# Kernel tuning notes

Hardware: AMD Instinct MI355X
Metric: run time of the kernel (lower is better)

Reference implementation:

```python
import jax, jax.numpy as jnp
import numpy as np

# 3D multi-scale deformable attention (MSDeformAttn, n_heads=8 / 3D variant)
LEVEL_SHAPES = [(32, 32, 32), (16, 16, 16), (8, 8, 8), (4, 4, 4)]  # (H, W, D) per level
D_MODEL, N_HEADS, N_LEVELS, N_POINTS = 256, 8, 4, 4
C_HEAD = D_MODEL // N_HEADS  # 32
N_BATCH, LEN_Q = 1, 37440
LEN_IN = sum(h * w * d for h, w, d in LEVEL_SHAPES)  # 37440


def setup_inputs() -> dict:
    key = jax.random.key(0)
    ks = jax.random.split(key, 10)
    s = 0.02  # param init scale
    return {
        "query": jax.random.normal(ks[0], (N_BATCH, LEN_Q, D_MODEL), jnp.float32),
        "reference_points": jax.random.uniform(ks[1], (N_BATCH, LEN_Q, N_LEVELS, 3), jnp.float32),
        "input_flatten": jax.random.normal(ks[2], (N_BATCH, LEN_IN, D_MODEL), jnp.float32),
        "input_spatial_shapes": jnp.array(LEVEL_SHAPES, dtype=jnp.int32),
        "input_level_start_index": jnp.array(
            np.cumsum([0] + [h * w * d for h, w, d in LEVEL_SHAPES])[:-1], dtype=jnp.int32),
        "W_value": s * jax.random.normal(ks[3], (D_MODEL, D_MODEL), jnp.float32),
        "b_value": jnp.zeros((D_MODEL,), jnp.float32),
        "W_off": s * jax.random.normal(ks[4], (D_MODEL, N_HEADS * N_LEVELS * N_POINTS * 3), jnp.float32),
        "b_off": s * jax.random.normal(ks[5], (N_HEADS * N_LEVELS * N_POINTS * 3,), jnp.float32),
        "W_attn": s * jax.random.normal(ks[6], (D_MODEL, N_HEADS * N_LEVELS * N_POINTS), jnp.float32),
        "b_attn": jnp.zeros((N_HEADS * N_LEVELS * N_POINTS,), jnp.float32),
        "W_out": s * jax.random.normal(ks[7], (D_MODEL, D_MODEL), jnp.float32),
        "b_out": jnp.zeros((D_MODEL,), jnp.float32),
    }


def trilinear_sample(vol, gx, gy, gz):
    """torch F.grid_sample 3D, mode=bilinear, padding=zeros, align_corners=False.
    vol: (B, C, Dz, Dy, Dx); gx indexes Dx, gy indexes Dy, gz indexes Dz, each (B, Q) in [-1,1].
    Returns (B, C, Q)."""
    B, C, Dz, Dy, Dx = vol.shape
    ix = ((gx + 1.0) * Dx - 1.0) * 0.5
    iy = ((gy + 1.0) * Dy - 1.0) * 0.5
    iz = ((gz + 1.0) * Dz - 1.0) * 0.5
    x0f, y0f, z0f = jnp.floor(ix), jnp.floor(iy), jnp.floor(iz)
    fx, fy, fz = ix - x0f, iy - y0f, iz - z0f
    x0, y0, z0 = x0f.astype(jnp.int32), y0f.astype(jnp.int32), z0f.astype(jnp.int32)
    vol_f = vol.reshape(B, C, Dz * Dy * Dx)
    out = jnp.zeros((B, C, gx.shape[1]), vol.dtype)
    for dz in (0, 1):
        for dy in (0, 1):
            for dx in (0, 1):
                xc, yc, zc = x0 + dx, y0 + dy, z0 + dz
                w = ((fx if dx else 1.0 - fx) * (fy if dy else 1.0 - fy) * (fz if dz else 1.0 - fz))
                valid = ((xc >= 0) & (xc < Dx) & (yc >= 0) & (yc < Dy) & (zc >= 0) & (zc < Dz))
                idx = (jnp.clip(zc, 0, Dz - 1) * Dy + jnp.clip(yc, 0, Dy - 1)) * Dx + jnp.clip(xc, 0, Dx - 1)
                v = jnp.take_along_axis(vol_f, idx[:, None, :], axis=2)  # (B, C, Q)
                out = out + (w * valid.astype(w.dtype))[:, None, :] * v
    return out


def reference(query, reference_points, input_flatten, input_spatial_shapes,
              input_level_start_index, W_value, b_value, W_off, b_off,
              W_attn, b_attn, W_out, b_out):
    N, Lq, _ = query.shape
    Lin = input_flatten.shape[1]
    value = (input_flatten @ W_value + b_value).reshape(N, Lin, N_HEADS, C_HEAD)
    off = (query @ W_off + b_off).reshape(N, Lq, N_HEADS, N_LEVELS, N_POINTS, 3)
    attn = jax.nn.softmax((query @ W_attn + b_attn).reshape(N, Lq, N_HEADS, N_LEVELS * N_POINTS), axis=-1)
    # offset_normalizer = [W, H, D] per level (as in the torch code)
    norm = jnp.stack([input_spatial_shapes[:, 1], input_spatial_shapes[:, 0],
                      input_spatial_shapes[:, 2]], -1).astype(query.dtype)
    loc = reference_points[:, :, None, :, None, :] + off / norm[None, None, None, :, None, :]
    grids = 2.0 * loc - 1.0  # (N, Lq, M, L, P, 3)
    starts = np.cumsum([0] + [h * w * d for h, w, d in LEVEL_SHAPES])
    sampled = []
    for l, (H, W, D) in enumerate(LEVEL_SHAPES):
        vl = value[:, starts[l]:starts[l + 1]]  # (N, H*W*D, M, C)
        vol = (vl.reshape(N, H, W, D, N_HEADS, C_HEAD)
                 .transpose(0, 4, 5, 1, 2, 3)
                 .reshape(N * N_HEADS, C_HEAD, H, W, D))
        g = grids[:, :, :, l].transpose(0, 2, 1, 3, 4).reshape(N * N_HEADS, Lq * N_POINTS, 3)
        # grid x indexes last vol dim (D), y indexes W, z indexes H (torch grid_sample convention)
        s = trilinear_sample(vol, g[..., 0], g[..., 1], g[..., 2])  # (N*M, C, Lq*P)
        sampled.append(s.reshape(N * N_HEADS, C_HEAD, Lq, N_POINTS))
    samp = jnp.stack(sampled, axis=-2).reshape(N * N_HEADS, C_HEAD, Lq, N_LEVELS * N_POINTS)
    aw = attn.transpose(0, 2, 1, 3).reshape(N * N_HEADS, 1, Lq, N_LEVELS * N_POINTS)
    out = (samp * aw).sum(-1).reshape(N, N_HEADS * C_HEAD, Lq).transpose(0, 2, 1)
    return out @ W_out + b_out
```

## Files before the change

### kernel.cpp

```cpp
#include <hip/hip_runtime.h>
#include <math.h>

#define LQ      37440
#define LIN     37440
#define DMODEL  256
#define NHEADS  8
#define CHEAD   32
#define K_DIM   256

typedef __attribute__((ext_vector_type(8))) short short8;
typedef __attribute__((ext_vector_type(4))) short short4v;
typedef __attribute__((ext_vector_type(4))) float f32x4;
typedef __attribute__((ext_vector_type(2))) float f32x2;

__device__ inline unsigned short bf16_rte(float f) {
    union { float f; unsigned u; } v; v.f = f;
    return (unsigned short)((v.u + 0x7fffu + ((v.u >> 16) & 1u)) >> 16);
}
__device__ inline float bf16_f(unsigned short s) {
    union { unsigned u; float f; } v; v.u = ((unsigned)s) << 16;
    return v.f;
}
__device__ inline float bits_f(unsigned u) {
    union { unsigned u; float f; } v; v.u = u;
    return v.f;
}
__device__ inline unsigned pkbf(float a, float b) {
    return (unsigned)bf16_rte(a) | ((unsigned)bf16_rte(b) << 16);
}

__global__ __launch_bounds__(256) void prep_all(
        const float* __restrict__ inp, const float* __restrict__ query,
        const float* __restrict__ Wv, const float* __restrict__ Wo,
        const float* __restrict__ Wa, const float* __restrict__ Wout,
        const float* __restrict__ bo, const float* __restrict__ ba,
        unsigned short* __restrict__ in_b, unsigned short* __restrict__ q_b,
        unsigned short* __restrict__ Bv, unsigned short* __restrict__ Bq,
        unsigned short* __restrict__ Bw, float* __restrict__ bias_m, int n4)
{
    const int bid = blockIdx.x;
    if (bid < 18720) {
        int i = bid * 256 + threadIdx.x;
        const float* src;
        unsigned short* dst;
        int j;
        if (i < n4) { src = inp;   dst = in_b; j = i; }
        else        { src = query; dst = q_b;  j = i - n4; }
        float4 v = ((const float4*)src)[j];
        short4v h;
        h.x = (short)bf16_rte(v.x);
        h.y = (short)bf16_rte(v.y);
        h.z = (short)bf16_rte(v.z);
        h.w = (short)bf16_rte(v.w);
        ((short4v*)dst)[j] = h;
    } else {
        int i = (bid - 18720) * 256 + threadIdx.x;
        int n = i >> 8, k = i & 255;
        if (n < 256) {
            Bv[(size_t)n * 256 + k] = bf16_rte(Wv[(size_t)k * 256 + n]);
        } else if (n < 640) {
            int m = n - 256;
            Bq[(size_t)m * 256 + k] = bf16_rte(Wo[(size_t)k * 384 + m]);
        } else if (n < 768) {
            int m = n - 640;
            Bq[(size_t)(384 + m) * 256 + k] = bf16_rte(Wa[(size_t)k * 128 + m]);
        } else {
            int m = n - 768;
            Bw[(size_t)m * 256 + k] = bf16_rte(Wout[(size_t)k * 256 + m]);
        }
        if (i < 512) bias_m[i] = (i < 384) ? bo[i] : ba[i - 384];
    }
}

__global__ __launch_bounds__(256) void gemm2(
    const unsigned short* __restrict__ in_b, const unsigned short* __restrict__ q_b,
    const unsigned short* __restrict__ Bv,   const unsigned short* __restrict__ Bq,
    const float* __restrict__ bv, const float* __restrict__ bias_m,
    unsigned short* __restrict__ value_t, unsigned short* __restrict__ qbuf)
{
    __shared__ __align__(16) unsigned short As[128][40];
    __shared__ __align__(16) unsigned short Bs[128][40];

    const int t    = threadIdx.x;
    const int bm   = blockIdx.y * 128;
    const int w    = t >> 6;
    const int lane = t & 63;
    const int lm   = lane & 15;
    const int quad = lane >> 4;

    const int isval = (blockIdx.x < 2);
    const unsigned short* A  = isval ? in_b : q_b;
    const unsigned short* Bt = isval ? Bv : Bq;
    const float* bias        = isval ? bv : bias_m;
    const int n0             = (isval ? blockIdx.x : (blockIdx.x - 2)) * 128;

    const int s_row = t >> 1;
    const int s_k   = (t & 1) << 4;

    int arow_g = bm + s_row; if (arow_g >= LQ) arow_g = LQ - 1;
    const size_t a_off = (size_t)arow_g * K_DIM + s_k;
    const size_t b_off = (size_t)(n0 + s_row) * K_DIM + s_k;

    f32x4 acc[2][8];
    #pragma unroll
    for (int mt = 0; mt < 2; ++mt)
        #pragma unroll
        for (int nt = 0; nt < 8; ++nt)
            acc[mt][nt] = (f32x4){0.f, 0.f, 0.f, 0.f};

    for (int k0 = 0; k0 < K_DIM; k0 += 32) {
        int4 a0 = *(const int4*)(A + a_off + k0);
        int4 a1 = *(const int4*)(A + a_off + k0 + 8);
        int4 b0 = *(const int4*)(Bt + b_off + k0);
        int4 b1 = *(const int4*)(Bt + b_off + k0 + 8);
        __syncthreads();
        *(int4*)&As[s_row][s_k]     = a0;
        *(int4*)&As[s_row][s_k + 8] = a1;
        *(int4*)&Bs[s_row][s_k]     = b0;
        *(int4*)&Bs[s_row][s_k + 8] = b1;
        __syncthreads();

        short8 af[2], bf[8];
        #pragma unroll
        for (int mt = 0; mt < 2; ++mt)
            af[mt] = *(const short8*)&As[w * 32 + mt * 16 + lm][quad * 8];
        #pragma unroll
        for (int nt = 0; nt < 8; ++nt)
            bf[nt] = *(const short8*)&Bs[nt * 16 + lm][quad * 8];
        #pragma unroll
        for (int mt = 0; mt < 2; ++mt)
            #pragma unroll
            for (int nt = 0; nt < 8; ++nt)
                acc[mt][nt] = __builtin_amdgcn_mfma_f32_16x16x32_bf16(af[mt], bf[nt], acc[mt][nt], 0, 0, 0);
    }

    #pragma unroll
    for (int nt = 0; nt < 8; ++nt) {
        int col = n0 + nt * 16 + lm;
        float bb = bias[col];
        #pragma unroll
        for (int mt = 0; mt < 2; ++mt)
            #pragma unroll
            for (int r = 0; r < 4; ++r) {
                int row = bm + w * 32 + mt * 16 + quad * 4 + r;
                if (row < LQ) {
                    float o = acc[mt][nt][r] + bb;
                    if (isval) {
                        int h = col >> 5, c = col & 31;
                        value_t[((size_t)h * LIN + row) * 32 + c] = bf16_rte(o);
                    } else {
                        qbuf[(size_t)row * 512 + col] = bf16_rte(o);
                    }
                }
            }
    }
}

__global__ __launch_bounds__(256) void gemm_out(
    const unsigned short* __restrict__ A, const unsigned short* __restrict__ Bt,
    const float* __restrict__ bias, float* __restrict__ Cout)
{
    __shared__ __align__(16) unsigned short As[128][40];
    __shared__ __align__(16) unsigned short Bs[128][40];

    const int t    = threadIdx.x;
    const int bm   = blockIdx.y * 128;
    const int n0   = blockIdx.x * 128;
    const int w    = t >> 6;
    const int lane = t & 63;
    const int lm   = lane & 15;
    const int quad = lane >> 4;

    const int s_row = t >> 1;
    const int s_k   = (t & 1) << 4;

    int arow_g = bm + s_row; if (arow_g >= LQ) arow_g = LQ - 1;
    const size_t a_off = (size_t)arow_g * K_DIM + s_k;
    const size_t b_off = (size_t)(n0 + s_row) * K_DIM + s_k;

    f32x4 acc[2][8];
    #pragma unroll
    for (int mt = 0; mt < 2; ++mt)
        #pragma unroll
        for (int nt = 0; nt < 8; ++nt)
            acc[mt][nt] = (f32x4){0.f, 0.f, 0.f, 0.f};

    for (int k0 = 0; k0 < K_DIM; k0 += 32) {
        int4 a0 = *(const int4*)(A + a_off + k0);
        int4 a1 = *(const int4*)(A + a_off + k0 + 8);
        int4 b0 = *(const int4*)(Bt + b_off + k0);
        int4 b1 = *(const int4*)(Bt + b_off + k0 + 8);
        __syncthreads();
        *(int4*)&As[s_row][s_k]     = a0;
        *(int4*)&As[s_row][s_k + 8] = a1;
        *(int4*)&Bs[s_row][s_k]     = b0;
        *(int4*)&Bs[s_row][s_k + 8] = b1;
        __syncthreads();

        short8 af[2], bf[8];
        #pragma unroll
        for (int mt = 0; mt < 2; ++mt)
            af[mt] = *(const short8*)&As[w * 32 + mt * 16 + lm][quad * 8];
        #pragma unroll
        for (int nt = 0; nt < 8; ++nt)
            bf[nt] = *(const short8*)&Bs[nt * 16 + lm][quad * 8];
        #pragma unroll
        for (int mt = 0; mt < 2; ++mt)
            #pragma unroll
            for (int nt = 0; nt < 8; ++nt)
                acc[mt][nt] = __builtin_amdgcn_mfma_f32_16x16x32_bf16(af[mt], bf[nt], acc[mt][nt], 0, 0, 0);
    }

    #pragma unroll
    for (int nt = 0; nt < 8; ++nt) {
        int col = n0 + nt * 16 + lm;
        float bb = bias[col];
        #pragma unroll
        for (int mt = 0; mt < 2; ++mt)
            #pragma unroll
            for (int r = 0; r < 4; ++r) {
                int row = bm + w * 32 + mt * 16 + quad * 4 + r;
                if (row < LQ)
                    Cout[(size_t)row * DMODEL + col] = acc[mt][nt][r] + bb;
            }
    }
}

__global__ __launch_bounds__(256) void sample_kernel(
    const float* __restrict__ refp,
    const unsigned short* __restrict__ qbuf,
    const unsigned short* __restrict__ value_t,
    unsigned short* __restrict__ samp)
{
    __shared__ float4 zywS[4][16][8];
    __shared__ f32x2  wxS [4][16][8];
    __shared__ int4   ozyS[4][16][8];
    __shared__ int    xbS [4][16][8];
    __shared__ float  lg  [4][128];

    const int t  = threadIdx.x;
    const int q0 = blockIdx.x * 4;

    const int   Sz[4]   = {32, 16, 8, 4};
    const float invS[4] = {1.f/32.f, 1.f/16.f, 1.f/8.f, 1.f/4.f};
    const int   St[4]   = {0, 32768, 36864, 37376};

    #pragma unroll
    for (int pi = t; pi < 512; pi += 256) {
        int ql = pi >> 7;
        int hp = pi & 127;
        int hh = hp >> 4;
        int c  = hp & 15;
        int l  = c >> 2;
        int q  = q0 + ql;
        const unsigned short* o = qbuf + (size_t)q * 512 + hp * 3;
        const float* r = refp + q * 12 + l * 3;
        const int   S  = Sz[l];
        const float Sf = (float)S;
        const float is = invS[l];
        float ix = (r[0] + bf16_f(o[0]) * is) * Sf - 0.5f;
        float iy = (r[1] + bf16_f(o[1]) * is) * Sf - 0.5f;
        float iz = (r[2] + bf16_f(o[2]) * is) * Sf - 0.5f;
        float xf = floorf(ix), yf = floorf(iy), zf = floorf(iz);
        float fx = ix - xf, fy = iy - yf, fz = iz - zf;
        int x0 = (int)xf, y0 = (int)yf, z0 = (int)zf;

        float wx0 = (x0 >= 0  && x0 < S)     ? (1.f - fx) : 0.f;
        float wx1 = (x0 >= -1 && x0 < S - 1) ? fx         : 0.f;
        float wy0 = (y0 >= 0  && y0 < S)     ? (1.f - fy) : 0.f;
        float wy1 = (y0 >= -1 && y0 < S - 1) ? fy         : 0.f;
        float wz0 = (z0 >= 0  && z0 < S)     ? (1.f - fz) : 0.f;
        float wz1 = (z0 >= -1 && z0 < S - 1) ? fz         : 0.f;

        int cy0 = min(max(y0, 0), S - 1), cy1 = min(max(y0 + 1, 0), S - 1);
        int cz0 = min(max(z0, 0), S - 1), cz1 = min(max(z0 + 1, 0), S - 1);

        const int S2 = S * S;
        const int st = St[l];
        zywS[ql][c][hh] = make_float4(wz0*wy0, wz0*wy1, wz1*wy0, wz1*wy1);
        wxS [ql][c][hh] = (f32x2){wx0, wx1};
        ozyS[ql][c][hh] = make_int4((st + cz0*S2 + cy0*S) * 32,
                                    (st + cz0*S2 + cy1*S) * 32,
                                    (st + cz1*S2 + cy0*S) * 32,
                                    (st + cz1*S2 + cy1*S) * 32);
        xbS [ql][c][hh] = x0 * 32;
        lg[ql][hp] = bf16_f(qbuf[(size_t)q * 512 + 384 + hp]);
    }
    __syncthreads();

    #pragma unroll
    for (int pi = t; pi < 512; pi += 256) {
        int ql = pi >> 7;
        int hp = pi & 127;
        int hh = hp >> 4;
        int c  = hp & 15;
        const float* L = &lg[ql][hh << 4];
        float m = L[0];
        #pragma unroll
        for (int j = 1; j < 16; ++j) m = fmaxf(m, L[j]);
        float s = 0.f;
        #pragma unroll
        for (int j = 0; j < 16; ++j) s += expf(L[j] - m);
        float a = expf(lg[ql][hp] - m) / s;
        f32x2 wv = wxS[ql][c][hh];
        wxS[ql][c][hh] = (f32x2){wv.x * a, wv.y * a};
    }
    __syncthreads();

    const int ql   = t >> 6;
    const int lane = t & 63;
    const int hh   = lane >> 3;
    const int j    = lane & 7;
    const int xsel = j >> 2;
    const int cgrp = (j & 3) << 3;
    const int q    = q0 + ql;

    const unsigned short* vbase = value_t - 64;
    const unsigned laneoff = (unsigned)(hh * (LIN * 32) + j * 8 + 64);

    f32x2 acc0 = {0.f,0.f}, acc1 = {0.f,0.f}, acc2 = {0.f,0.f}, acc3 = {0.f,0.f};

    #pragma unroll
    for (int c = 0; c < 16; ++c) {
        float4 zyw = zywS[ql][c][hh];
        f32x2  wx  = wxS [ql][c][hh];
        int4   zo  = ozyS[ql][c][hh];
        int    xb  = xbS [ql][c][hh];
        float  ws  = xsel ? wx.y : wx.x;
        const unsigned pb = laneoff + (unsigned)xb;

        #define CORNER(OFF, WZ) { \
            int4 v = *(const int4*)(vbase + (unsigned)(pb + (unsigned)(OFF))); \
            float w_ = (WZ) * ws; \
            f32x2 w2 = {w_, w_}; \
            acc0 += w2 * (f32x2){bits_f(((unsigned)v.x) << 16), bits_f((unsigned)v.x)}; \
            acc1 += w2 * (f32x2){bits_f(((unsigned)v.y) << 16), bits_f((unsigned)v.y)}; \
            acc2 += w2 * (f32x2){bits_f(((unsigned)v.z) << 16), bits_f((unsigned)v.z)}; \
            acc3 += w2 * (f32x2){bits_f(((unsigned)v.w) << 16), bits_f((unsigned)v.w)}; }

        CORNER(zo.x, zyw.x);
        CORNER(zo.y, zyw.y);
        CORNER(zo.z, zyw.z);
        CORNER(zo.w, zyw.w);
        #undef CORNER
    }

    float c0 = acc0.x + __shfl_xor(acc0.x, 4);
    float c1 = acc0.y + __shfl_xor(acc0.y, 4);
    float c2 = acc1.x + __shfl_xor(acc1.x, 4);
    float c3 = acc1.y + __shfl_xor(acc1.y, 4);
    float c4 = acc2.x + __shfl_xor(acc2.x, 4);
    float c5 = acc2.y + __shfl_xor(acc2.y, 4);
    float c6 = acc3.x + __shfl_xor(acc3.x, 4);
    float c7 = acc3.y + __shfl_xor(acc3.y, 4);
    if (xsel == 0) {
        int4 o = make_int4((int)pkbf(c0, c1), (int)pkbf(c2, c3),
                           (int)pkbf(c4, c5), (int)pkbf(c6, c7));
        *(int4*)(samp + (size_t)q * DMODEL + hh * CHEAD + cgrp) = o;
    }
}

extern "C" void kernel_launch(void* const* d_in, const int* in_sizes, int n_in,
                              void* d_out, int out_size, void* d_ws, size_t ws_size,
                              hipStream_t stream) {
    const float* query = (const float*)d_in[0];
    const float* refp  = (const float*)d_in[1];
    const float* inp   = (const float*)d_in[2];
    const float* Wv   = (const float*)d_in[5];
    const float* bv   = (const float*)d_in[6];
    const float* Wo   = (const float*)d_in[7];
    const float* bo   = (const float*)d_in[8];
    const float* Wa   = (const float*)d_in[9];
    const float* ba   = (const float*)d_in[10];
    const float* Wout = (const float*)d_in[11];
    const float* bout = (const float*)d_in[12];

    char* p = (char*)d_ws;
    p += 256;
    unsigned short* value_t = (unsigned short*)p; p += (size_t)LIN * 256 * 2;
    unsigned short* qbuf    = (unsigned short*)p; p += (size_t)LQ * 512 * 2;
    unsigned short* samp    = (unsigned short*)p; p += (size_t)LQ * 256 * 2;
    unsigned short* in_b    = (unsigned short*)p; p += (size_t)LQ * 256 * 2;
    unsigned short* q_b     = (unsigned short*)p; p += (size_t)LQ * 256 * 2;
    unsigned short* Bv   = (unsigned short*)p;    p += 256 * 256 * 2;
    unsigned short* Bq   = (unsigned short*)p;    p += 512 * 256 * 2;
    unsigned short* Bw   = (unsigned short*)p;    p += 256 * 256 * 2;
    float* bias_m = (float*)p;                    p += 512 * 4;

    const int n4 = LQ * 256 / 4;
    dim3 blk(256);

    prep_all<<<18720 + 1024, blk, 0, stream>>>(
        inp, query, Wv, Wo, Wa, Wout, bo, ba,
        in_b, q_b, Bv, Bq, Bw, bias_m, n4);
    gemm2<<<dim3(6, (LQ + 127) / 128), blk, 0, stream>>>(
        in_b, q_b, Bv, Bq, bv, bias_m, value_t, qbuf);
    sample_kernel<<<LQ / 4, blk, 0, stream>>>(refp, qbuf, value_t, samp);
    gemm_out<<<dim3(2, (LQ + 127) / 128), blk, 0, stream>>>(samp, Bw, bout, (float*)d_out);
}
```

Measured before the change: 353.3 us.

## Use direct global-to-LDS loads with swizzle in GEMMs and fuse softmax via shuffles

```diff
diff --git a/kernel.cpp b/kernel.cpp
--- a/kernel.cpp
+++ b/kernel.cpp
@@ -27,6 +27,12 @@
 }
 __device__ inline unsigned pkbf(float a, float b) {
     return (unsigned)bf16_rte(a) | ((unsigned)bf16_rte(b) << 16);
+}
+
+__device__ __forceinline__ void gl_lds16(const unsigned short* g, unsigned short* l) {
+    __builtin_amdgcn_global_load_lds(
+        (const __attribute__((address_space(1))) void*)g,
+        (__attribute__((address_space(3))) void*)l, 16, 0, 0);
 }
 
 __global__ __launch_bounds__(256) void prep_all(
@@ -78,8 +84,8 @@
     const float* __restrict__ bv, const float* __restrict__ bias_m,
     unsigned short* __restrict__ value_t, unsigned short* __restrict__ qbuf)
 {
-    __shared__ __align__(16) unsigned short As[128][40];
-    __shared__ __align__(16) unsigned short Bs[128][40];
+    __shared__ __align__(16) unsigned short AsL[128 * 32];
+    __shared__ __align__(16) unsigned short BsL[128 * 32];
 
     const int t    = threadIdx.x;
     const int bm   = blockIdx.y * 128;
@@ -94,12 +100,29 @@
     const float* bias        = isval ? bv : bias_m;
     const int n0             = (isval ? blockIdx.x : (blockIdx.x - 2)) * 128;
 
-    const int s_row = t >> 1;
-    const int s_k   = (t & 1) << 4;
-
-    int arow_g = bm + s_row; if (arow_g >= LQ) arow_g = LQ - 1;
-    const size_t a_off = (size_t)arow_g * K_DIM + s_k;
-    const size_t b_off = (size_t)(n0 + s_row) * K_DIM + s_k;
+    const unsigned short* ga[2]; unsigned short* la[2];
+    const unsigned short* gb[2]; unsigned short* lb[2];
+    #pragma unroll
+    for (int i = 0; i < 2; ++i) {
+        int idx = i * 256 + t;
+        int row = idx >> 2;
+        int chn = (idx & 3) ^ ((row >> 1) & 3);
+        int rga = bm + row; if (rga >= LQ) rga = LQ - 1;
+        ga[i] = A  + (size_t)rga * K_DIM + chn * 8;
+        gb[i] = Bt + (size_t)(n0 + row) * K_DIM + chn * 8;
+        la[i] = AsL + i * 2048 + (t >> 6) * 512;
+        lb[i] = BsL + i * 2048 + (t >> 6) * 512;
+    }
+
+    const int ra0 = w * 32 + lm, ra1 = ra0 + 16;
+    const int aoff0 = ra0 * 32 + ((quad ^ ((ra0 >> 1) & 3)) << 3);
+    const int aoff1 = ra1 * 32 + ((quad ^ ((ra1 >> 1) & 3)) << 3);
+    int boff[8];
+    #pragma unroll
+    for (int nt = 0; nt < 8; ++nt) {
+        int rb = nt * 16 + lm;
+        boff[nt] = rb * 32 + ((quad ^ ((rb >> 1) & 3)) << 3);
+    }
 
     f32x4 acc[2][8];
     #pragma unroll
@@ -109,24 +132,19 @@
             acc[mt][nt] = (f32x4){0.f, 0.f, 0.f, 0.f};
 
     for (int k0 = 0; k0 < K_DIM; k0 += 32) {
-        int4 a0 = *(const int4*)(A + a_off + k0);
-        int4 a1 = *(const int4*)(A + a_off + k0 + 8);
-        int4 b0 = *(const int4*)(Bt + b_off + k0);
-        int4 b1 = *(const int4*)(Bt + b_off + k0 + 8);
         __syncthreads();
-        *(int4*)&As[s_row][s_k]     = a0;
-        *(int4*)&As[s_row][s_k + 8] = a1;
-        *(int4*)&Bs[s_row][s_k]     = b0;
-        *(int4*)&Bs[s_row][s_k + 8] = b1;
+        gl_lds16(ga[0] + k0, la[0]);
+        gl_lds16(ga[1] + k0, la[1]);
+        gl_lds16(gb[0] + k0, lb[0]);
+        gl_lds16(gb[1] + k0, lb[1]);
         __syncthreads();
 
         short8 af[2], bf[8];
-        #pragma unroll
-        for (int mt = 0; mt < 2; ++mt)
-            af[mt] = *(const short8*)&As[w * 32 + mt * 16 + lm][quad * 8];
+        af[0] = *(const short8*)&AsL[aoff0];
+        af[1] = *(const short8*)&AsL[aoff1];
         #pragma unroll
         for (int nt = 0; nt < 8; ++nt)
-            bf[nt] = *(const short8*)&Bs[nt * 16 + lm][quad * 8];
+            bf[nt] = *(const short8*)&BsL[boff[nt]];
         #pragma unroll
         for (int mt = 0; mt < 2; ++mt)
             #pragma unroll
@@ -160,8 +178,8 @@
     const unsigned short* __restrict__ A, const unsigned short* __restrict__ Bt,
     const float* __restrict__ bias, float* __restrict__ Cout)
 {
-    __shared__ __align__(16) unsigned short As[128][40];
-    __shared__ __align__(16) unsigned short Bs[128][40];
+    __shared__ __align__(16) unsigned short AsL[128 * 32];
+    __shared__ __align__(16) unsigned short BsL[128 * 32];
 
     const int t    = threadIdx.x;
     const int bm   = blockIdx.y * 128;
@@ -171,12 +189,29 @@
     const int lm   = lane & 15;
     const int quad = lane >> 4;
 
-    const int s_row = t >> 1;
-    const int s_k   = (t & 1) << 4;
-
-    int arow_g = bm + s_row; if (arow_g >= LQ) arow_g = LQ - 1;
-    const size_t a_off = (size_t)arow_g * K_DIM + s_k;
-    const size_t b_off = (size_t)(n0 + s_row) * K_DIM + s_k;
+    const unsigned short* ga[2]; unsigned short* la[2];
+    const unsigned short* gb[2]; unsigned short* lb[2];
+    #pragma unroll
+    for (int i = 0; i < 2; ++i) {
+        int idx = i * 256 + t;
+        int row = idx >> 2;
+        int chn = (idx & 3) ^ ((row >> 1) & 3);
+        int rga = bm + row; if (rga >= LQ) rga = LQ - 1;
+        ga[i] = A  + (size_t)rga * K_DIM + chn * 8;
+        gb[i] = Bt + (size_t)(n0 + row) * K_DIM + chn * 8;
+        la[i] = AsL + i * 2048 + (t >> 6) * 512;
+        lb[i] = BsL + i * 2048 + (t >> 6) * 512;
+    }
+
+    const int ra0 = w * 32 + lm, ra1 = ra0 + 16;
+    const int aoff0 = ra0 * 32 + ((quad ^ ((ra0 >> 1) & 3)) << 3);
+    const int aoff1 = ra1 * 32 + ((quad ^ ((ra1 >> 1) & 3)) << 3);
+    int boff[8];
+    #pragma unroll
+    for (int nt = 0; nt < 8; ++nt) {
+        int rb = nt * 16 + lm;
+        boff[nt] = rb * 32 + ((quad ^ ((rb >> 1) & 3)) << 3);
+    }
 
     f32x4 acc[2][8];
     #pragma unroll
@@ -186,24 +221,19 @@
             acc[mt][nt] = (f32x4){0.f, 0.f, 0.f, 0.f};
 
     for (int k0 = 0; k0 < K_DIM; k0 += 32) {
-        int4 a0 = *(const int4*)(A + a_off + k0);
-        int4 a1 = *(const int4*)(A + a_off + k0 + 8);
-        int4 b0 = *(const int4*)(Bt + b_off + k0);
-        int4 b1 = *(const int4*)(Bt + b_off + k0 + 8);
         __syncthreads();
-        *(int4*)&As[s_row][s_k]     = a0;
-        *(int4*)&As[s_row][s_k + 8] = a1;
-        *(int4*)&Bs[s_row][s_k]     = b0;
-        *(int4*)&Bs[s_row][s_k + 8] = b1;
+        gl_lds16(ga[0] + k0, la[0]);
+        gl_lds16(ga[1] + k0, la[1]);
+        gl_lds16(gb[0] + k0, lb[0]);
+        gl_lds16(gb[1] + k0, lb[1]);
         __syncthreads();
 
         short8 af[2], bf[8];
-        #pragma unroll
-        for (int mt = 0; mt < 2; ++mt)
-            af[mt] = *(const short8*)&As[w * 32 + mt * 16 + lm][quad * 8];
+        af[0] = *(const short8*)&AsL[aoff0];
+        af[1] = *(const short8*)&AsL[aoff1];
         #pragma unroll
         for (int nt = 0; nt < 8; ++nt)
-            bf[nt] = *(const short8*)&Bs[nt * 16 + lm][quad * 8];
+            bf[nt] = *(const short8*)&BsL[boff[nt]];
         #pragma unroll
         for (int mt = 0; mt < 2; ++mt)
             #pragma unroll
@@ -235,8 +265,6 @@
     __shared__ float4 zywS[4][16][8];
     __shared__ f32x2  wxS [4][16][8];
     __shared__ int4   ozyS[4][16][8];
-    __shared__ int    xbS [4][16][8];
-    __shared__ float  lg  [4][128];
 
     const int t  = threadIdx.x;
     const int q0 = blockIdx.x * 4;
@@ -275,35 +303,27 @@
         int cy0 = min(max(y0, 0), S - 1), cy1 = min(max(y0 + 1, 0), S - 1);
         int cz0 = min(max(z0, 0), S - 1), cz1 = min(max(z0 + 1, 0), S - 1);
 
+        float lgv = bf16_f(qbuf[(size_t)q * 512 + 384 + hp]);
+        float m = fmaxf(lgv, __shfl_xor(lgv, 1));
+        m = fmaxf(m, __shfl_xor(m, 2));
+        m = fmaxf(m, __shfl_xor(m, 4));
+        m = fmaxf(m, __shfl_xor(m, 8));
+        float e = __expf(lgv - m);
+        float s = e + __shfl_xor(e, 1);
+        s += __shfl_xor(s, 2);
+        s += __shfl_xor(s, 4);
+        s += __shfl_xor(s, 8);
+        float a = __fdividef(e, s);
+
         const int S2 = S * S;
         const int st = St[l];
+        const int xb = x0 * 32;
         zywS[ql][c][hh] = make_float4(wz0*wy0, wz0*wy1, wz1*wy0, wz1*wy1);
-        wxS [ql][c][hh] = (f32x2){wx0, wx1};
-        ozyS[ql][c][hh] = make_int4((st + cz0*S2 + cy0*S) * 32,
-                                    (st + cz0*S2 + cy1*S) * 32,
-                                    (st + cz1*S2 + cy0*S) * 32,
-                                    (st + cz1*S2 + cy1*S) * 32);
-        xbS [ql][c][hh] = x0 * 32;
-        lg[ql][hp] = bf16_f(qbuf[(size_t)q * 512 + 384 + hp]);
-    }
-    __syncthreads();
-
-    #pragma unroll
-    for (int pi = t; pi < 512; pi += 256) {
-        int ql = pi >> 7;
-        int hp = pi & 127;
-        int hh = hp >> 4;
-        int c  = hp & 15;
-        const float* L = &lg[ql][hh << 4];
-        float m = L[0];
-        #pragma unroll
-        for (int j = 1; j < 16; ++j) m = fmaxf(m, L[j]);
-        float s = 0.f;
-        #pragma unroll
-        for (int j = 0; j < 16; ++j) s += expf(L[j] - m);
-        float a = expf(lg[ql][hp] - m) / s;
-        f32x2 wv = wxS[ql][c][hh];
-        wxS[ql][c][hh] = (f32x2){wv.x * a, wv.y * a};
+        wxS [ql][c][hh] = (f32x2){wx0 * a, wx1 * a};
+        ozyS[ql][c][hh] = make_int4((st + cz0*S2 + cy0*S) * 32 + xb,
+                                    (st + cz0*S2 + cy1*S) * 32 + xb,
+                                    (st + cz1*S2 + cy0*S) * 32 + xb,
+                                    (st + cz1*S2 + cy1*S) * 32 + xb);
     }
     __syncthreads();
 
@@ -325,12 +345,10 @@
         float4 zyw = zywS[ql][c][hh];
         f32x2  wx  = wxS [ql][c][hh];
         int4   zo  = ozyS[ql][c][hh];
-        int    xb  = xbS [ql][c][hh];
         float  ws  = xsel ? wx.y : wx.x;
-        const unsigned pb = laneoff + (unsigned)xb;
 
         #define CORNER(OFF, WZ) { \
-            int4 v = *(const int4*)(vbase + (unsigned)(pb + (unsigned)(OFF))); \
+            int4 v = *(const int4*)(vbase + (laneoff + (unsigned)(OFF))); \
             float w_ = (WZ) * ws; \
             f32x2 w2 = {w_, w_}; \
             acc0 += w2 * (f32x2){bits_f(((unsigned)v.x) << 16), bits_f((unsigned)v.x)}; \
```

Measured after the change: 348.8 us. No clear change (-1.3%).
